# Performance work log

Measured on AMD Instinct MI355X. Metric: run time of the kernel, lower is better.

The kernel has to match this reference:

```python
import jax, jax.numpy as jnp
import numpy as np

N = 100000
E = 1000000
NODE_DIM = 128
EDGE_DIM = 32
HID = 64
HIER = 32
NUM_CLASS = 10
NUM_LAYERS = 3
BN_EPS = 1e-5


def setup_inputs() -> dict:
    key = jax.random.key(0)
    ks = jax.random.split(key, 16)
    s = 0.05
    return {
        "x": jax.random.normal(ks[0], (N, NODE_DIM), jnp.float32),
        "e": jax.random.normal(ks[1], (E, EDGE_DIM), jnp.float32),
        "c": jax.random.normal(ks[2], (N, HIER), jnp.float32),
        "w_node": jax.random.normal(ks[3], (NODE_DIM, HID), jnp.float32) * s,
        "b_node": jnp.zeros((HID,), jnp.float32),
        "w_edge": jax.random.normal(ks[4], (EDGE_DIM, HID), jnp.float32) * s,
        "b_edge": jnp.zeros((HID,), jnp.float32),
        "w_out1": jax.random.normal(ks[5], (HIER + HID, 2 * HID), jnp.float32) * s,
        "b_out1": jnp.zeros((2 * HID,), jnp.float32),
        "bn_gamma": jnp.ones((2 * HID,), jnp.float32),
        "bn_beta": jnp.zeros((2 * HID,), jnp.float32),
        "prelu_a": jnp.asarray(0.25, jnp.float32),
        "w_out2": jax.random.normal(ks[6], (2 * HID, NUM_CLASS), jnp.float32) * s,
        "b_out2": jnp.zeros((NUM_CLASS,), jnp.float32),
        "edge_index": jax.random.randint(ks[7], (2, E), 0, N, jnp.int64),
    }


def reference(x, e, c, w_node, b_node, w_edge, b_edge, w_out1, b_out1,
              bn_gamma, bn_beta, prelu_a, w_out2, b_out2, edge_index):
    n = x.shape[0]
    h = x @ w_node + b_node                      # [N, HID]
    eh = e @ w_edge + b_edge                     # [E, HID]
    src, dst = edge_index[0], edge_index[1]
    loop = jnp.arange(n)
    # add_self_loops + zero self-loop edge_attr (done inside each GCN layer,
    # identical every layer so hoisted)
    src_f = jnp.concatenate([src, loop])
    dst_f = jnp.concatenate([dst, loop])
    e_f = jnp.concatenate([eh, jnp.zeros((n, eh.shape[1]), eh.dtype)], axis=0)
    deg = jax.ops.segment_sum(jnp.ones(dst_f.shape, x.dtype), dst_f, num_segments=n)
    dinv = deg ** -0.5                           # deg >= 1 thanks to self loops
    norm = (dinv[src_f] * dinv[dst_f])[:, None]  # [E+N, 1]
    h_sum = h
    for _ in range(NUM_LAYERS):
        msg = norm * (h[src_f] + e_f)            # gather + edge compute
        h = jax.ops.segment_sum(msg, dst_f, num_segments=n)  # scatter-add
        h = jax.nn.leaky_relu(h, 0.2)
        h_sum = h_sum + h                        # sum over h_list
    z = jnp.concatenate([h_sum, c], axis=-1) @ w_out1 + b_out1
    # BatchNorm1d (training-mode batch statistics, biased variance)
    mu = z.mean(axis=0)
    var = z.var(axis=0)
    z = (z - mu) / jnp.sqrt(var + BN_EPS) * bn_gamma + bn_beta
    z = jnp.where(z > 0, z, prelu_a * z)         # PReLU (single param)
    return z @ w_out2 + b_out2
```

## Files before the change

kernel.cpp:

```cpp
#include <hip/hip_runtime.h>
#include <math.h>

#define N_NODES 100000
#define N_EDGES 1000000
#define HID     64
#define HIER    32
#define NDIM    128
#define EDIM    32
#define K1      96
#define C1      128
#define NCLS    10
#define BN_EPS  1e-5f
#define SCAN_B  98
#define ZT64    1563
#define HTILES2 782

__device__ __forceinline__ unsigned pk_bf16(float a, float b) {
    unsigned ua = __float_as_uint(a);
    ua = (ua + 0x7FFFu + ((ua >> 16) & 1u)) >> 16;
    unsigned ub = __float_as_uint(b);
    ub = (ub + 0x7FFFu + ((ub >> 16) & 1u)) & 0xFFFF0000u;
    return ua | ub;
}
__device__ __forceinline__ float bf_lo(unsigned g) { return __uint_as_float(g << 16); }
__device__ __forceinline__ float bf_hi(unsigned g) { return __uint_as_float(g & 0xFFFF0000u); }


__global__ void k_count(const int* __restrict__ ei, int* __restrict__ cnt) {
    int i = blockIdx.x * blockDim.x + threadIdx.x;
    if (i < N_EDGES) atomicAdd(&cnt[ei[N_EDGES + i]], 1);
}

__global__ void k_scan1(const int* __restrict__ cnt, int* __restrict__ offs,
                        float* __restrict__ dinv, int* __restrict__ bsum) {
    __shared__ int buf[2][1024];
    int t = threadIdx.x, b = blockIdx.x;
    int i = b * 1024 + t;
    int v = (i < N_NODES) ? cnt[i] : 0;
    buf[0][t] = v; __syncthreads();
    int pi = 0;
    for (int off = 1; off < 1024; off <<= 1) {
        int x = buf[pi][t];
        if (t >= off) x += buf[pi][t - off];
        buf[pi ^ 1][t] = x; __syncthreads(); pi ^= 1;
    }
    int incl = buf[pi][t];
    if (i < N_NODES) {
        offs[i] = incl - v;
        dinv[i] = rsqrtf((float)(v + 1));
    }
    if (t == 1023) bsum[b] = incl;
}

__global__ void k_scan2(int* __restrict__ bsum, int nb) {
    __shared__ int buf[2][1024];
    int t = threadIdx.x;
    int v = (t < nb) ? bsum[t] : 0;
    buf[0][t] = v; __syncthreads();
    int pi = 0;
    for (int off = 1; off < 1024; off <<= 1) {
        int x = buf[pi][t];
        if (t >= off) x += buf[pi][t - off];
        buf[pi ^ 1][t] = x; __syncthreads(); pi ^= 1;
    }
    int incl = buf[pi][t];
    if (t < nb) bsum[t] = incl - v;
}

__global__ void k_scan3(const int* __restrict__ bsum, int* __restrict__ offs) {
    int b = blockIdx.x;
    int i = b * 1024 + threadIdx.x;
    if (i < N_NODES) offs[i] += bsum[b];
    if (i == 0) offs[N_NODES] = N_EDGES;
}

__global__ void k_fill(const int* __restrict__ ei, const int* __restrict__ offs,
                       int* __restrict__ cursor, const float* __restrict__ dinv,
                       uint2* __restrict__ epk) {
    int i = blockIdx.x * blockDim.x + threadIdx.x;
    if (i >= N_EDGES) return;
    int s = ei[i], d = ei[N_EDGES + i];
    int pos = offs[d] + atomicAdd(&cursor[d], 1);
    unsigned nhi = pk_bf16(dinv[s], 0.f) << 16;
    epk[pos] = make_uint2((unsigned)i | ((unsigned)(s & 0xFFF) << 20),
                          nhi | (unsigned)(s >> 12));
}


__global__ __launch_bounds__(256) void k_conv(const float4* __restrict__ e4,
                                              uint4* __restrict__ eb4) {
    int i = blockIdx.x * 256 + threadIdx.x;
    float4 a = e4[(size_t)2 * i];
    float4 b = e4[(size_t)2 * i + 1];
    uint4 pk;
    pk.x = pk_bf16(a.x, a.y); pk.y = pk_bf16(a.z, a.w);
    pk.z = pk_bf16(b.x, b.y); pk.w = pk_bf16(b.z, b.w);
    eb4[i] = pk;
}

__global__ __launch_bounds__(256) void k_conv2(const float4* __restrict__ c4,
                                               uint2* __restrict__ cb2) {
    int i = blockIdx.x * 256 + threadIdx.x;
    if (i >= N_NODES * 8) return;
    float4 a = c4[i];
    cb2[i] = make_uint2(pk_bf16(a.x, a.y), pk_bf16(a.z, a.w));
}


__global__ __launch_bounds__(256) void k_agg3(const unsigned* __restrict__ ebfu,
                                              const uint2* __restrict__ epk,
                                              const int* __restrict__ offs,
                                              const float* __restrict__ dinv,
                                              float* __restrict__ agg,
                                              float* __restrict__ wsumv) {
    int v = (blockIdx.x * 256 + threadIdx.x) >> 4;
    if (v >= N_NODES) return;
    int q = threadIdx.x & 15;
    int start = offs[v], end = offs[v + 1];
    float ax = 0.f, ay = 0.f, wacc = 0.f;
    for (int i = start; i < end; i += 4) {
        int i1 = i + 1, i2 = i + 2, i3 = i + 3;
        uint2 p0 = epk[i];
        uint2 p1 = (i1 < end) ? epk[i1] : make_uint2(0u, 0u);
        uint2 p2 = (i2 < end) ? epk[i2] : make_uint2(0u, 0u);
        uint2 p3 = (i3 < end) ? epk[i3] : make_uint2(0u, 0u);
        float n0 = bf_hi(p0.y), n1 = bf_hi(p1.y);
        float n2 = bf_hi(p2.y), n3 = bf_hi(p3.y);
        unsigned g0 = ebfu[(size_t)(p0.x & 0xFFFFFu) * 16 + q];
        unsigned g1 = ebfu[(size_t)(p1.x & 0xFFFFFu) * 16 + q];
        unsigned g2 = ebfu[(size_t)(p2.x & 0xFFFFFu) * 16 + q];
        unsigned g3 = ebfu[(size_t)(p3.x & 0xFFFFFu) * 16 + q];
        ax += n0 * bf_lo(g0) + n1 * bf_lo(g1) + n2 * bf_lo(g2) + n3 * bf_lo(g3);
        ay += n0 * bf_hi(g0) + n1 * bf_hi(g1) + n2 * bf_hi(g2) + n3 * bf_hi(g3);
        wacc += n0 + n1 + n2 + n3;
    }
    float dv = dinv[v];
    *(float2*)&agg[(size_t)v * EDIM + q * 2] = make_float2(dv * ax, dv * ay);
    if (q == 0) wsumv[v] = dv * wacc;
}


__global__ __launch_bounds__(256) void k_h0t2(const float* __restrict__ x,
                                              const float* __restrict__ w,
                                              const float* __restrict__ bias,
                                              unsigned* __restrict__ hbf) {
    __shared__ __align__(16) unsigned wpk[NDIM * 36];
    __shared__ float xt[128 * 33];
    for (int i = threadIdx.x; i < NDIM * 32; i += 256) {
        int k = i >> 5, j = i & 31;
        wpk[k * 36 + j] = pk_bf16(w[k * HID + 2 * j], w[k * HID + 2 * j + 1]);
    }
    int tid = threadIdx.x;
    int lane = tid & 63, wave = tid >> 6;
    int lr = lane >> 3, lc = lane & 7;
    int rbase = wave * 32 + lr * 4;
    int cbase = lc * 8;
    float bA[8];
    #pragma unroll
    for (int j = 0; j < 8; ++j) bA[j] = bias[cbase + j];
    for (int tile = blockIdx.x; tile < HTILES2; tile += gridDim.x) {
        int row0 = tile * 128;
        float acc[4][8];
        #pragma unroll
        for (int i = 0; i < 4; ++i)
            #pragma unroll
            for (int j = 0; j < 8; ++j) acc[i][j] = 0.f;
        for (int ch = 0; ch < 4; ++ch) {
            __syncthreads();
            #pragma unroll
            for (int p = 0; p < 4; ++p) {
                int idx = p * 256 + tid;
                int row = idx >> 3, kq = idx & 7;
                int gk = ch * 32 + kq * 4;
                float4 v = make_float4(0.f, 0.f, 0.f, 0.f);
                int gr = row0 + row;
                if (gr < N_NODES) v = *(const float4*)&x[(size_t)gr * NDIM + gk];
                float* d = &xt[row * 33 + kq * 4];
                d[0] = v.x; d[1] = v.y; d[2] = v.z; d[3] = v.w;
            }
            __syncthreads();
            for (int k = 0; k < 32; ++k) {
                float u[4];
                #pragma unroll
                for (int i = 0; i < 4; ++i) u[i] = xt[(rbase + i) * 33 + k];
                uint4 wp = *(const uint4*)&wpk[(ch * 32 + k) * 36 + lc * 4];
                float wv[8];
                wv[0] = bf_lo(wp.x); wv[1] = bf_hi(wp.x);
                wv[2] = bf_lo(wp.y); wv[3] = bf_hi(wp.y);
                wv[4] = bf_lo(wp.z); wv[5] = bf_hi(wp.z);
                wv[6] = bf_lo(wp.w); wv[7] = bf_hi(wp.w);
                #pragma unroll
                for (int i = 0; i < 4; ++i)
                    #pragma unroll
                    for (int j = 0; j < 8; ++j) acc[i][j] += u[i] * wv[j];
            }
        }
        #pragma unroll
        for (int i = 0; i < 4; ++i) {
            int gr = row0 + rbase + i;
            if (gr < N_NODES) {
                uint4 pk;
                pk.x = pk_bf16(acc[i][0] + bA[0], acc[i][1] + bA[1]);
                pk.y = pk_bf16(acc[i][2] + bA[2], acc[i][3] + bA[3]);
                pk.z = pk_bf16(acc[i][4] + bA[4], acc[i][5] + bA[5]);
                pk.w = pk_bf16(acc[i][6] + bA[6], acc[i][7] + bA[7]);
                *(uint4*)&hbf[(size_t)gr * 32 + (cbase >> 1)] = pk;
            }
        }
    }
}


__global__ __launch_bounds__(256) void k_se(const float* __restrict__ agg,
                                            const float* __restrict__ wsumv,
                                            const float* __restrict__ we,
                                            const float* __restrict__ be,
                                            unsigned* __restrict__ sebf) {
    int lane = threadIdx.x & 63, wid = threadIdx.x >> 6;
    float wreg[EDIM];
    #pragma unroll
    for (int k = 0; k < EDIM; ++k) wreg[k] = we[k * HID + lane];
    float bl = be[lane];
    for (int v = blockIdx.x * 4 + wid; v < N_NODES; v += gridDim.x * 4) {
        const float4* ar = (const float4*)(agg + (size_t)v * EDIM);
        float acc = wsumv[v] * bl;
        #pragma unroll
        for (int k4 = 0; k4 < EDIM / 4; ++k4) {
            float4 av = ar[k4];
            int k = k4 * 4;
            acc += av.x * wreg[k + 0] + av.y * wreg[k + 1] +
                   av.z * wreg[k + 2] + av.w * wreg[k + 3];
        }
        float partner = __shfl_xor(acc, 1);
        if ((lane & 1) == 0)
            sebf[(size_t)v * 32 + (lane >> 1)] = pk_bf16(acc, partner);
    }
}


__device__ __forceinline__ int dec_src(uint2 p) {
    return (int)(((p.y & 0xFFFFu) << 12) | (p.x >> 20));
}

__global__ __launch_bounds__(256) void k_layer4(const unsigned* __restrict__ hold,
                                                const unsigned* __restrict__ sebf,
                                                const uint2* __restrict__ epk,
                                                const int* __restrict__ offs,
                                                const float* __restrict__ dinv,
                                                unsigned* __restrict__ hnew) {
    int v = (blockIdx.x * 256 + threadIdx.x) >> 4;
    if (v >= N_NODES) return;
    int q = threadIdx.x & 15;
    int start = offs[v], end = offs[v + 1];
    float dv = dinv[v];
    size_t vp = (size_t)v * 16 + q;
    uint2 hv = ((const uint2*)hold)[vp];
    float a0 = dv * bf_lo(hv.x), a1 = dv * bf_hi(hv.x);
    float a2 = dv * bf_lo(hv.y), a3 = dv * bf_hi(hv.y);
    for (int i = start; i < end; i += 8) {
        int idx[8]; float nn[8]; uint2 gg[8];
        #pragma unroll
        for (int u = 0; u < 8; ++u) {
            int ii = i + u;
            uint2 p = (ii < end) ? epk[ii] : make_uint2(0u, 0u);
            idx[u] = dec_src(p);
            nn[u]  = bf_hi(p.y);
        }
        #pragma unroll
        for (int u = 0; u < 8; ++u) gg[u] = ((const uint2*)hold)[(size_t)idx[u] * 16 + q];
        #pragma unroll
        for (int u = 0; u < 8; ++u) {
            a0 += nn[u] * bf_lo(gg[u].x); a1 += nn[u] * bf_hi(gg[u].x);
            a2 += nn[u] * bf_lo(gg[u].y); a3 += nn[u] * bf_hi(gg[u].y);
        }
    }
    uint2 sv = ((const uint2*)sebf)[vp];
    float r0 = bf_lo(sv.x) + dv * a0;
    float r1 = bf_hi(sv.x) + dv * a1;
    float r2 = bf_lo(sv.y) + dv * a2;
    float r3 = bf_hi(sv.y) + dv * a3;
    r0 = (r0 > 0.f) ? r0 : 0.2f * r0;
    r1 = (r1 > 0.f) ? r1 : 0.2f * r1;
    r2 = (r2 > 0.f) ? r2 : 0.2f * r2;
    r3 = (r3 > 0.f) ? r3 : 0.2f * r3;
    ((uint2*)hnew)[vp] = make_uint2(pk_bf16(r0, r1), pk_bf16(r2, r3));
}

__global__ __launch_bounds__(256) void k_layer4s(const unsigned* __restrict__ hold,
                                                 const unsigned* __restrict__ hb0,
                                                 const unsigned* __restrict__ hb1,
                                                 const unsigned* __restrict__ sebf,
                                                 const uint2* __restrict__ epk,
                                                 const int* __restrict__ offs,
                                                 const float* __restrict__ dinv,
                                                 unsigned* __restrict__ hnew,
                                                 unsigned* __restrict__ hsbf) {
    int v = (blockIdx.x * 256 + threadIdx.x) >> 4;
    if (v >= N_NODES) return;
    int q = threadIdx.x & 15;
    int start = offs[v], end = offs[v + 1];
    float dv = dinv[v];
    size_t vp = (size_t)v * 16 + q;
    uint2 hv = ((const uint2*)hold)[vp];
    float a0 = dv * bf_lo(hv.x), a1 = dv * bf_hi(hv.x);
    float a2 = dv * bf_lo(hv.y), a3 = dv * bf_hi(hv.y);
    for (int i = start; i < end; i += 8) {
        int idx[8]; float nn[8]; uint2 gg[8];
        #pragma unroll
        for (int u = 0; u < 8; ++u) {
            int ii = i + u;
            uint2 p = (ii < end) ? epk[ii] : make_uint2(0u, 0u);
            idx[u] = dec_src(p);
            nn[u]  = bf_hi(p.y);
        }
        #pragma unroll
        for (int u = 0; u < 8; ++u) gg[u] = ((const uint2*)hold)[(size_t)idx[u] * 16 + q];
        #pragma unroll
        for (int u = 0; u < 8; ++u) {
            a0 += nn[u] * bf_lo(gg[u].x); a1 += nn[u] * bf_hi(gg[u].x);
            a2 += nn[u] * bf_lo(gg[u].y); a3 += nn[u] * bf_hi(gg[u].y);
        }
    }
    uint2 sv = ((const uint2*)sebf)[vp];
    float r0 = bf_lo(sv.x) + dv * a0;
    float r1 = bf_hi(sv.x) + dv * a1;
    float r2 = bf_lo(sv.y) + dv * a2;
    float r3 = bf_hi(sv.y) + dv * a3;
    r0 = (r0 > 0.f) ? r0 : 0.2f * r0;
    r1 = (r1 > 0.f) ? r1 : 0.2f * r1;
    r2 = (r2 > 0.f) ? r2 : 0.2f * r2;
    r3 = (r3 > 0.f) ? r3 : 0.2f * r3;
    ((uint2*)hnew)[vp] = make_uint2(pk_bf16(r0, r1), pk_bf16(r2, r3));
    uint2 g0 = ((const uint2*)hb0)[vp];
    uint2 g1 = ((const uint2*)hb1)[vp];
    float s0 = r0 + bf_lo(g0.x) + bf_lo(g1.x) + bf_lo(hv.x);
    float s1 = r1 + bf_hi(g0.x) + bf_hi(g1.x) + bf_hi(hv.x);
    float s2 = r2 + bf_lo(g0.y) + bf_lo(g1.y) + bf_lo(hv.y);
    float s3 = r3 + bf_hi(g0.y) + bf_hi(g1.y) + bf_hi(hv.y);
    ((uint2*)hsbf)[vp] = make_uint2(pk_bf16(s0, s1), pk_bf16(s2, s3));
}


__global__ __launch_bounds__(256) void k_zstats(const unsigned* __restrict__ hsbf,
                                                const unsigned* __restrict__ cbf,
                                                const float* __restrict__ w1,
                                                const float* __restrict__ b1,
                                                unsigned* __restrict__ zbf,
                                                float* __restrict__ stats) {
    __shared__ __align__(16) unsigned wpk[K1 * 64];
    __shared__ __align__(16) unsigned ut[K1 * 36];
    __shared__ float red[4][64];
    for (int i = threadIdx.x; i < K1 * 64; i += 256) {
        int k = i >> 6, j = i & 63;
        wpk[i] = pk_bf16(w1[k * C1 + 2 * j], w1[k * C1 + 2 * j + 1]);
    }
    int tid = threadIdx.x;
    int lane = tid & 63, wave = tid >> 6;
    int lr = lane >> 3, lc = lane & 7;
    int wr = wave >> 1, wc = wave & 1;
    int rbase = wr * 32 + lr * 4;
    int cbase = wc * 64 + lc * 8;
    int rp_st = tid & 31, kslot = tid >> 5;
    float bA[8];
    #pragma unroll
    for (int j = 0; j < 8; ++j) bA[j] = b1[cbase + j];
    float s[8], q[8];
    #pragma unroll
    for (int j = 0; j < 8; ++j) { s[j] = 0.f; q[j] = 0.f; }

    for (int tile = blockIdx.x; tile < ZT64; tile += gridDim.x) {
        int row0 = tile * 64;
        __syncthreads();
        {
            int r0g = row0 + 2 * rp_st, r1g = r0g + 1;
            bool ok0 = r0g < N_NODES, ok1 = r1g < N_NODES;
            #pragma unroll
            for (int kku = 0; kku < 6; ++kku) {
                int ku = kslot * 6 + kku;
                unsigned A = 0u, B = 0u;
                if (ku < 32) {
                    if (ok0) A = hsbf[(size_t)r0g * 32 + ku];
                    if (ok1) B = hsbf[(size_t)r1g * 32 + ku];
                } else {
                    if (ok0) A = cbf[(size_t)r0g * 16 + (ku - 32)];
                    if (ok1) B = cbf[(size_t)r1g * 16 + (ku - 32)];
                }
                int k0 = 2 * ku;
                ut[k0 * 36 + rp_st]       = (A & 0xFFFFu) | (B << 16);
                ut[(k0 + 1) * 36 + rp_st] = (A >> 16) | (B & 0xFFFF0000u);
            }
        }
        __syncthreads();
        float acc[4][8];
        #pragma unroll
        for (int i = 0; i < 4; ++i)
            #pragma unroll
            for (int j = 0; j < 8; ++j) acc[i][j] = 0.f;
        for (int k = 0; k < K1; ++k) {
            uint2 up = *(const uint2*)&ut[k * 36 + wr * 16 + lr * 2];
            uint4 wp = *(const uint4*)&wpk[k * 64 + wc * 32 + lc * 4];
            float u[4], wv[8];
            u[0] = bf_lo(up.x); u[1] = bf_hi(up.x);
            u[2] = bf_lo(up.y); u[3] = bf_hi(up.y);
            wv[0] = bf_lo(wp.x); wv[1] = bf_hi(wp.x);
            wv[2] = bf_lo(wp.y); wv[3] = bf_hi(wp.y);
            wv[4] = bf_lo(wp.z); wv[5] = bf_hi(wp.z);
            wv[6] = bf_lo(wp.w); wv[7] = bf_hi(wp.w);
            #pragma unroll
            for (int i = 0; i < 4; ++i) {
                acc[i][0] += u[i] * wv[0]; acc[i][1] += u[i] * wv[1];
                acc[i][2] += u[i] * wv[2]; acc[i][3] += u[i] * wv[3];
                acc[i][4] += u[i] * wv[4]; acc[i][5] += u[i] * wv[5];
                acc[i][6] += u[i] * wv[6]; acc[i][7] += u[i] * wv[7];
            }
        }
        #pragma unroll
        for (int i = 0; i < 4; ++i) {
            int gr = row0 + rbase + i;
            if (gr < N_NODES) {
                float zz[8];
                #pragma unroll
                for (int j = 0; j < 8; ++j) {
                    zz[j] = acc[i][j] + bA[j];
                    s[j] += zz[j]; q[j] += zz[j] * zz[j];
                }
                uint4 pk;
                pk.x = pk_bf16(zz[0], zz[1]); pk.y = pk_bf16(zz[2], zz[3]);
                pk.z = pk_bf16(zz[4], zz[5]); pk.w = pk_bf16(zz[6], zz[7]);
                *(uint4*)&zbf[(size_t)gr * 64 + (cbase >> 1)] = pk;
            }
        }
    }

    #pragma unroll
    for (int j = 0; j < 8; ++j) {
        s[j] += __shfl_xor(s[j], 8); s[j] += __shfl_xor(s[j], 16); s[j] += __shfl_xor(s[j], 32);
        q[j] += __shfl_xor(q[j], 8); q[j] += __shfl_xor(q[j], 16); q[j] += __shfl_xor(q[j], 32);
    }
    __syncthreads();
    if (lr == 0) {
        #pragma unroll
        for (int j = 0; j < 8; ++j) red[wave][lc * 8 + j] = s[j];
    }
    __syncthreads();
    if (tid < 128) {
        int wc2 = tid >> 6, cl = tid & 63;
        atomicAdd(&stats[wc2 * 64 + cl], red[wc2][cl] + red[wc2 + 2][cl]);
    }
    __syncthreads();
    if (lr == 0) {
        #pragma unroll
        for (int j = 0; j < 8; ++j) red[wave][lc * 8 + j] = q[j];
    }
    __syncthreads();
    if (tid < 128) {
        int wc2 = tid >> 6, cl = tid & 63;
        atomicAdd(&stats[C1 + wc2 * 64 + cl], red[wc2][cl] + red[wc2 + 2][cl]);
    }
}

__global__ void k_ab(const float* __restrict__ stats, const float* __restrict__ gamma,
                     const float* __restrict__ beta, float* __restrict__ ab) {
    int t = threadIdx.x;
    if (t < C1) {
        float mu = stats[t] / (float)N_NODES;
        float var = stats[C1 + t] / (float)N_NODES - mu * mu;
        float inv = rsqrtf(var + BN_EPS);
        float a = gamma[t] * inv;
        ab[t] = a;
        ab[C1 + t] = beta[t] - mu * a;
    }
}


__global__ __launch_bounds__(256) void k_out3(const unsigned* __restrict__ zbf,
                                              const float* __restrict__ ab,
                                              const float* __restrict__ pa,
                                              const float* __restrict__ w2,
                                              const float* __restrict__ b2,
                                              float* __restrict__ out) {
    int v = blockIdx.x * 256 + threadIdx.x;
    if (v >= N_NODES) return;
    float alpha = pa[0];
    float acc[NCLS];
    #pragma unroll
    for (int j = 0; j < NCLS; ++j) acc[j] = b2[j];
    const uint4* zr = (const uint4*)(zbf + (size_t)v * 64);
    #pragma unroll
    for (int pk4 = 0; pk4 < 16; ++pk4) {
        uint4 g = zr[pk4];
        unsigned gw[4] = {g.x, g.y, g.z, g.w};
        #pragma unroll
        for (int w = 0; w < 4; ++w) {
            int d0 = pk4 * 8 + w * 2;
            float p0 = bf_lo(gw[w]) * ab[d0]     + ab[C1 + d0];
            float p1 = bf_hi(gw[w]) * ab[d0 + 1] + ab[C1 + d0 + 1];
            p0 = (p0 > 0.f) ? p0 : alpha * p0;
            p1 = (p1 > 0.f) ? p1 : alpha * p1;
            #pragma unroll
            for (int j = 0; j < NCLS; ++j)
                acc[j] += p0 * w2[d0 * NCLS + j] + p1 * w2[(d0 + 1) * NCLS + j];
        }
    }
    #pragma unroll
    for (int j = 0; j < NCLS; ++j) out[(size_t)v * NCLS + j] = acc[j];
}


extern "C" void kernel_launch(void* const* d_in, const int* in_sizes, int n_in,
                              void* d_out, int out_size, void* d_ws, size_t ws_size,
                              hipStream_t stream) {
    const float* x      = (const float*)d_in[0];
    const float* e      = (const float*)d_in[1];
    const float* c      = (const float*)d_in[2];
    const float* w_node = (const float*)d_in[3];
    const float* b_node = (const float*)d_in[4];
    const float* w_edge = (const float*)d_in[5];
    const float* b_edge = (const float*)d_in[6];
    const float* w_out1 = (const float*)d_in[7];
    const float* b_out1 = (const float*)d_in[8];
    const float* gamma  = (const float*)d_in[9];
    const float* beta   = (const float*)d_in[10];
    const float* pa     = (const float*)d_in[11];
    const float* w_out2 = (const float*)d_in[12];
    const float* b_out2 = (const float*)d_in[13];
    const int*   ei     = (const int*)d_in[14];
    float* out = (float*)d_out;

    char* wsb = (char*)d_ws;
    ushort*   ebf  = (ushort*)wsb;
    unsigned* sebf = (unsigned*)wsb;
    unsigned* zbf  = (unsigned*)(wsb + 12800000);
    size_t off = (64000000 + 255) & ~(size_t)255;
    auto alloc = [&](size_t bytes) {
        void* p = wsb + off;
        off = (off + bytes + 255) & ~(size_t)255;
        return p;
    };
    int*      cnt      = (int*)alloc(4ull * N_NODES);
    int*      offs     = (int*)alloc(4ull * (N_NODES + 1));
    float*    dinv     = (float*)alloc(4ull * N_NODES);
    int*      bsum     = (int*)alloc(4ull * 128);
    uint2*    epk      = (uint2*)alloc(8ull * N_EDGES);
    float*    agg      = (float*)alloc(4ull * N_NODES * EDIM);
    float*    wsumv    = (float*)alloc(4ull * N_NODES);
    float*    stats    = (float*)alloc(4ull * 256);
    float*    ab       = (float*)alloc(4ull * 256);
    unsigned* hb0      = (unsigned*)alloc(4ull * N_NODES * 32);
    unsigned* hb1      = (unsigned*)alloc(4ull * N_NODES * 32);
    unsigned* hb2      = (unsigned*)alloc(4ull * N_NODES * 32);
    unsigned* hb3      = (unsigned*)alloc(4ull * N_NODES * 32);
    unsigned* cbf      = (unsigned*)alloc(4ull * N_NODES * 16);
    unsigned* hsbf     = (unsigned*)agg;

    hipMemsetAsync(cnt, 0, 4ull * N_NODES, stream);
    hipMemsetAsync(stats, 0, 4ull * 256, stream);

    k_count<<<(N_EDGES + 255) / 256, 256, 0, stream>>>(ei, cnt);
    k_scan1<<<SCAN_B, 1024, 0, stream>>>(cnt, offs, dinv, bsum);
    k_scan2<<<1, 1024, 0, stream>>>(bsum, SCAN_B);
    k_scan3<<<SCAN_B, 1024, 0, stream>>>(bsum, offs);
    hipMemsetAsync(cnt, 0, 4ull * N_NODES, stream);
    k_fill<<<(N_EDGES + 255) / 256, 256, 0, stream>>>(ei, offs, cnt, dinv, epk);

    k_conv<<<15625, 256, 0, stream>>>((const float4*)e, (uint4*)ebf);
    k_agg3<<<N_NODES * 16 / 256, 256, 0, stream>>>((const unsigned*)ebf, epk,
                                                   offs, dinv, agg, wsumv);

    k_se<<<1280, 256, 0, stream>>>(agg, wsumv, w_edge, b_edge, sebf);
    k_conv2<<<(N_NODES * 8 + 255) / 256, 256, 0, stream>>>((const float4*)c, (uint2*)cbf);
    k_h0t2<<<HTILES2, 256, 0, stream>>>(x, w_node, b_node, hb0);

    k_layer4<<<N_NODES * 16 / 256, 256, 0, stream>>>(hb0, sebf, epk, offs, dinv, hb1);
    k_layer4<<<N_NODES * 16 / 256, 256, 0, stream>>>(hb1, sebf, epk, offs, dinv, hb2);
    k_layer4s<<<N_NODES * 16 / 256, 256, 0, stream>>>(hb2, hb0, hb1, sebf, epk, offs,
                                                      dinv, hb3, hsbf);

    k_zstats<<<ZT64, 256, 0, stream>>>(hsbf, cbf, w_out1, b_out1, zbf, stats);
    k_ab<<<1, 128, 0, stream>>>(stats, gamma, beta, ab);
    k_out3<<<(N_NODES + 255) / 256, 256, 0, stream>>>(zbf, ab, pa, w_out2, b_out2, out);
}
```

Before: 443.8 us.

## Compute output projection and BN stats with bf16 MFMA instead of scalar FMA

Replaces the shared-memory tiled scalar-FMA GEMM for the [N,96]x[96,128] output projection with a kernel where each wave computes a 16-row strip using 16x16x32 bf16 MFMA instructions, loading A fragments straight from global memory. The weights are prepacked into MFMA B-fragment layout once by a small new kernel, instead of every block repacking them into LDS. Per-column sum and sum-of-squares for BatchNorm are still reduced in-wave and atomically added per block. Output stores are now 4-byte scattered writes paired via shuffles rather than 16-byte vector stores, which may cost some write efficiency.

After: 432.0 us. 2.6% less time.

```diff
diff --git a/kernel.cpp b/kernel.cpp
--- a/kernel.cpp
+++ b/kernel.cpp
@@ -12,8 +12,11 @@
 #define NCLS    10
 #define BN_EPS  1e-5f
 #define SCAN_B  98
-#define ZT64    1563
 #define HTILES2 782
+#define ZSTRIPS 6250
+
+typedef __attribute__((ext_vector_type(8))) short short8;
+typedef __attribute__((ext_vector_type(4))) float f32x4;
 
 __device__ __forceinline__ unsigned pk_bf16(float a, float b) {
     unsigned ua = __float_as_uint(a);
@@ -24,6 +27,9 @@
 }
 __device__ __forceinline__ float bf_lo(unsigned g) { return __uint_as_float(g << 16); }
 __device__ __forceinline__ float bf_hi(unsigned g) { return __uint_as_float(g & 0xFFFF0000u); }
+__device__ __forceinline__ short8 as_s8(uint4 u) {
+    union { uint4 u; short8 s; } c; c.u = u; return c.s;
+}
 
 
 __global__ void k_count(const int* __restrict__ ei, int* __restrict__ cnt) {
@@ -104,6 +110,19 @@
     if (i >= N_NODES * 8) return;
     float4 a = c4[i];
     cb2[i] = make_uint2(pk_bf16(a.x, a.y), pk_bf16(a.z, a.w));
+}
+
+__global__ __launch_bounds__(256) void k_wpack(const float* __restrict__ w1,
+                                               uint4* __restrict__ bpkg) {
+    int i = blockIdx.x * 256 + threadIdx.x;
+    if (i >= 12 * C1) return;
+    int g = i >> 7, n = i & 127;
+    uint4 r;
+    r.x = pk_bf16(w1[(8 * g + 0) * C1 + n], w1[(8 * g + 1) * C1 + n]);
+    r.y = pk_bf16(w1[(8 * g + 2) * C1 + n], w1[(8 * g + 3) * C1 + n]);
+    r.z = pk_bf16(w1[(8 * g + 4) * C1 + n], w1[(8 * g + 5) * C1 + n]);
+    r.w = pk_bf16(w1[(8 * g + 6) * C1 + n], w1[(8 * g + 7) * C1 + n]);
+    bpkg[i] = r;
 }
 
 
@@ -341,121 +360,65 @@
 }
 
 
-__global__ __launch_bounds__(256) void k_zstats(const unsigned* __restrict__ hsbf,
-                                                const unsigned* __restrict__ cbf,
-                                                const float* __restrict__ w1,
-                                                const float* __restrict__ b1,
-                                                unsigned* __restrict__ zbf,
-                                                float* __restrict__ stats) {
-    __shared__ __align__(16) unsigned wpk[K1 * 64];
-    __shared__ __align__(16) unsigned ut[K1 * 36];
-    __shared__ float red[4][64];
-    for (int i = threadIdx.x; i < K1 * 64; i += 256) {
-        int k = i >> 6, j = i & 63;
-        wpk[i] = pk_bf16(w1[k * C1 + 2 * j], w1[k * C1 + 2 * j + 1]);
-    }
+__global__ __launch_bounds__(256) void k_zmfma(const unsigned* __restrict__ hsbf,
+                                               const unsigned* __restrict__ cbf,
+                                               const uint4* __restrict__ bpkg,
+                                               const float* __restrict__ b1,
+                                               unsigned* __restrict__ zbf,
+                                               float* __restrict__ stats) {
+    __shared__ float red[2][4][C1];
     int tid = threadIdx.x;
-    int lane = tid & 63, wave = tid >> 6;
-    int lr = lane >> 3, lc = lane & 7;
-    int wr = wave >> 1, wc = wave & 1;
-    int rbase = wr * 32 + lr * 4;
-    int cbase = wc * 64 + lc * 8;
-    int rp_st = tid & 31, kslot = tid >> 5;
-    float bA[8];
-    #pragma unroll
-    for (int j = 0; j < 8; ++j) bA[j] = b1[cbase + j];
-    float s[8], q[8];
-    #pragma unroll
-    for (int j = 0; j < 8; ++j) { s[j] = 0.f; q[j] = 0.f; }
-
-    for (int tile = blockIdx.x; tile < ZT64; tile += gridDim.x) {
-        int row0 = tile * 64;
-        __syncthreads();
-        {
-            int r0g = row0 + 2 * rp_st, r1g = r0g + 1;
-            bool ok0 = r0g < N_NODES, ok1 = r1g < N_NODES;
-            #pragma unroll
-            for (int kku = 0; kku < 6; ++kku) {
-                int ku = kslot * 6 + kku;
-                unsigned A = 0u, B = 0u;
-                if (ku < 32) {
-                    if (ok0) A = hsbf[(size_t)r0g * 32 + ku];
-                    if (ok1) B = hsbf[(size_t)r1g * 32 + ku];
-                } else {
-                    if (ok0) A = cbf[(size_t)r0g * 16 + (ku - 32)];
-                    if (ok1) B = cbf[(size_t)r1g * 16 + (ku - 32)];
-                }
-                int k0 = 2 * ku;
-                ut[k0 * 36 + rp_st]       = (A & 0xFFFFu) | (B << 16);
-                ut[(k0 + 1) * 36 + rp_st] = (A >> 16) | (B & 0xFFFF0000u);
-            }
-        }
-        __syncthreads();
-        float acc[4][8];
-        #pragma unroll
-        for (int i = 0; i < 4; ++i)
-            #pragma unroll
-            for (int j = 0; j < 8; ++j) acc[i][j] = 0.f;
-        for (int k = 0; k < K1; ++k) {
-            uint2 up = *(const uint2*)&ut[k * 36 + wr * 16 + lr * 2];
-            uint4 wp = *(const uint4*)&wpk[k * 64 + wc * 32 + lc * 4];
-            float u[4], wv[8];
-            u[0] = bf_lo(up.x); u[1] = bf_hi(up.x);
-            u[2] = bf_lo(up.y); u[3] = bf_hi(up.y);
-            wv[0] = bf_lo(wp.x); wv[1] = bf_hi(wp.x);
-            wv[2] = bf_lo(wp.y); wv[3] = bf_hi(wp.y);
-            wv[4] = bf_lo(wp.z); wv[5] = bf_hi(wp.z);
-            wv[6] = bf_lo(wp.w); wv[7] = bf_hi(wp.w);
+    int wave = tid >> 6, lane = tid & 63;
+    int l15 = lane & 15, lg = lane >> 4;
+    int strip = blockIdx.x * 4 + wave;
+    float sN[8], qN[8];
+    #pragma unroll
+    for (int j = 0; j < 8; ++j) { sN[j] = 0.f; qN[j] = 0.f; }
+    if (strip < ZSTRIPS) {
+        int row = strip * 16 + l15;
+        short8 A0 = as_s8(*(const uint4*)&hsbf[(size_t)row * 32 + lg * 4]);
+        short8 A1 = as_s8(*(const uint4*)&hsbf[(size_t)row * 32 + 16 + lg * 4]);
+        short8 A2 = as_s8(*(const uint4*)&cbf[(size_t)row * 16 + lg * 4]);
+        int rb = strip * 16 + lg * 4;
+        #pragma unroll
+        for (int ct = 0; ct < 8; ++ct) {
+            int n = ct * 16 + l15;
+            short8 B0 = as_s8(bpkg[lg * C1 + n]);
+            short8 B1 = as_s8(bpkg[(4 + lg) * C1 + n]);
+            short8 B2 = as_s8(bpkg[(8 + lg) * C1 + n]);
+            f32x4 acc = {0.f, 0.f, 0.f, 0.f};
+            acc = __builtin_amdgcn_mfma_f32_16x16x32_bf16(A0, B0, acc, 0, 0, 0);
+            acc = __builtin_amdgcn_mfma_f32_16x16x32_bf16(A1, B1, acc, 0, 0, 0);
+            acc = __builtin_amdgcn_mfma_f32_16x16x32_bf16(A2, B2, acc, 0, 0, 0);
+            float bias = b1[n];
             #pragma unroll
             for (int i = 0; i < 4; ++i) {
-                acc[i][0] += u[i] * wv[0]; acc[i][1] += u[i] * wv[1];
-                acc[i][2] += u[i] * wv[2]; acc[i][3] += u[i] * wv[3];
-                acc[i][4] += u[i] * wv[4]; acc[i][5] += u[i] * wv[5];
-                acc[i][6] += u[i] * wv[6]; acc[i][7] += u[i] * wv[7];
+                float zz = acc[i] + bias;
+                sN[ct] += zz; qN[ct] += zz * zz;
+                float pz = __shfl_xor(zz, 1);
+                if ((l15 & 1) == 0)
+                    zbf[(size_t)(rb + i) * 64 + (n >> 1)] = pk_bf16(zz, pz);
             }
         }
-        #pragma unroll
-        for (int i = 0; i < 4; ++i) {
-            int gr = row0 + rbase + i;
-            if (gr < N_NODES) {
-                float zz[8];
-                #pragma unroll
-                for (int j = 0; j < 8; ++j) {
-                    zz[j] = acc[i][j] + bA[j];
-                    s[j] += zz[j]; q[j] += zz[j] * zz[j];
-                }
-                uint4 pk;
-                pk.x = pk_bf16(zz[0], zz[1]); pk.y = pk_bf16(zz[2], zz[3]);
-                pk.z = pk_bf16(zz[4], zz[5]); pk.w = pk_bf16(zz[6], zz[7]);
-                *(uint4*)&zbf[(size_t)gr * 64 + (cbase >> 1)] = pk;
-            }
-        }
-    }
-
+    }
     #pragma unroll
     for (int j = 0; j < 8; ++j) {
-        s[j] += __shfl_xor(s[j], 8); s[j] += __shfl_xor(s[j], 16); s[j] += __shfl_xor(s[j], 32);
-        q[j] += __shfl_xor(q[j], 8); q[j] += __shfl_xor(q[j], 16); q[j] += __shfl_xor(q[j], 32);
+        sN[j] += __shfl_xor(sN[j], 16); sN[j] += __shfl_xor(sN[j], 32);
+        qN[j] += __shfl_xor(qN[j], 16); qN[j] += __shfl_xor(qN[j], 32);
+    }
+    if (lane < 16) {
+        #pragma unroll
+        for (int ct = 0; ct < 8; ++ct) {
+            red[0][wave][ct * 16 + lane] = sN[ct];
+            red[1][wave][ct * 16 + lane] = qN[ct];
+        }
     }
     __syncthreads();
-    if (lr == 0) {
-        #pragma unroll
-        for (int j = 0; j < 8; ++j) red[wave][lc * 8 + j] = s[j];
-    }
-    __syncthreads();
-    if (tid < 128) {
-        int wc2 = tid >> 6, cl = tid & 63;
-        atomicAdd(&stats[wc2 * 64 + cl], red[wc2][cl] + red[wc2 + 2][cl]);
-    }
-    __syncthreads();
-    if (lr == 0) {
-        #pragma unroll
-        for (int j = 0; j < 8; ++j) red[wave][lc * 8 + j] = q[j];
-    }
-    __syncthreads();
-    if (tid < 128) {
-        int wc2 = tid >> 6, cl = tid & 63;
-        atomicAdd(&stats[C1 + wc2 * 64 + cl], red[wc2][cl] + red[wc2 + 2][cl]);
+    if (tid < C1) {
+        atomicAdd(&stats[tid],
+                  red[0][0][tid] + red[0][1][tid] + red[0][2][tid] + red[0][3][tid]);
+        atomicAdd(&stats[C1 + tid],
+                  red[1][0][tid] + red[1][1][tid] + red[1][2][tid] + red[1][3][tid]);
     }
 }
 
@@ -551,6 +514,7 @@
     unsigned* hb2      = (unsigned*)alloc(4ull * N_NODES * 32);
     unsigned* hb3      = (unsigned*)alloc(4ull * N_NODES * 32);
     unsigned* cbf      = (unsigned*)alloc(4ull * N_NODES * 16);
+    uint4*    bpkg     = (uint4*)alloc(16ull * 12 * C1);
     unsigned* hsbf     = (unsigned*)agg;
 
     hipMemsetAsync(cnt, 0, 4ull * N_NODES, stream);
@@ -563,6 +527,7 @@
     hipMemsetAsync(cnt, 0, 4ull * N_NODES, stream);
     k_fill<<<(N_EDGES + 255) / 256, 256, 0, stream>>>(ei, offs, cnt, dinv, epk);
 
+    k_wpack<<<6, 256, 0, stream>>>(w_out1, bpkg);
     k_conv<<<15625, 256, 0, stream>>>((const float4*)e, (uint4*)ebf);
     k_agg3<<<N_NODES * 16 / 256, 256, 0, stream>>>((const unsigned*)ebf, epk,
                                                    offs, dinv, agg, wsumv);
@@ -576,7 +541,7 @@
     k_layer4s<<<N_NODES * 16 / 256, 256, 0, stream>>>(hb2, hb0, hb1, sebf, epk, offs,
                                                       dinv, hb3, hsbf);
 
-    k_zstats<<<ZT64, 256, 0, stream>>>(hsbf, cbf, w_out1, b_out1, zbf, stats);
+    k_zmfma<<<(ZSTRIPS + 3) / 4, 256, 0, stream>>>(hsbf, cbf, bpkg, b_out1, zbf, stats);
     k_ab<<<1, 128, 0, stream>>>(stats, gamma, beta, ab);
     k_out3<<<(N_NODES + 255) / 256, 256, 0, stream>>>(zbf, ab, pa, w_out2, b_out2, out);
 }
```
